# Performance work log

Hardware: AMD Instinct MI355X
Metric: run time of the kernel (lower is better)

## Reference

```python
import jax, jax.numpy as jnp
import numpy as np

DIM = 64
LEN = 256


def setup_inputs() -> dict:
    key = jax.random.key(0)
    ks = jax.random.split(key, 9)
    b, h, B = 4, 8, 16
    q = jax.random.normal(ks[0], (b, h, B, LEN, DIM), dtype=jnp.float32)
    k = jax.random.normal(ks[1], (b, h, B, LEN, DIM), dtype=jnp.float32)
    s = 1.0 / np.sqrt(DIM)
    Wq = jax.random.normal(ks[2], (1, DIM), dtype=jnp.float32) * s
    bq = jnp.ones((1,), dtype=jnp.float32)
    Wk = jax.random.normal(ks[3], (1, DIM), dtype=jnp.float32) * s
    bk = jnp.ones((1,), dtype=jnp.float32)
    sl = 1.0 / np.sqrt(LEN)
    W1 = jax.random.normal(ks[4], (1, LEN), dtype=jnp.float32) * sl
    W2a = jax.random.normal(ks[5], (LEN, LEN), dtype=jnp.float32) * sl
    W2b = jax.random.normal(ks[6], (1, LEN), dtype=jnp.float32) * sl
    return {"q": q, "k": k, "Wq": Wq, "bq": bq, "Wk": Wk, "bk": bk,
            "W1": W1, "W2a": W2a, "W2b": W2b}


def reference(q, k, Wq, bq, Wk, bk, W1, W2a, W2b):
    # Sigma_q/k: [b,h,B,L,1]
    Sigma_q = jnp.einsum('bhgid,od->bhgio', q, Wq) + bq
    Sigma_k = jnp.einsum('bhgjd,od->bhgjo', k, Wk) + bk
    # similarity: [b,h,B,L,L]
    sim = jnp.einsum('bhgid,bhgjd->bhgij', q, k)
    # outer product of the scalar projections: [b,h,B,L,L]
    Sigma = Sigma_q * jnp.swapaxes(Sigma_k, -1, -2)
    # zero the diagonal (sim - diag_embed(diag(sim)))
    eye = jnp.eye(sim.shape[-1], dtype=sim.dtype)
    sim_norm = sim * (1.0 - eye)
    # mlp1: Linear(L,1) over last axis -> [b,h,B,L]
    theta = jnp.einsum('bhgij,j->bhgi', sim_norm, W1[0])
    # mlp2: Linear(L,L) -> LeakyReLU(0.1) -> Linear(L,1) over axis i -> [b,h,B,1]
    hdn = jnp.einsum('bhgi,oi->bhgo', theta, W2a)
    hdn = jnp.where(hdn >= 0, hdn, 0.1 * hdn)
    theta = jnp.einsum('bhgi,oi->bhgo', hdn, W2b)[..., None]  # [b,h,B,1,1]
    sim = sim * Sigma
    attn = jax.nn.softmax(sim, axis=-1) * (sim > theta)
    return attn
```

## Files before the change

kernel.cpp:

```cpp
#include <hip/hip_runtime.h>
#include <math.h>

#define LL 256
#define DD 64

typedef __attribute__((ext_vector_type(8))) short bf16x8;
typedef __attribute__((ext_vector_type(4))) float f32x4;

static __device__ __forceinline__ unsigned short f2bf(float f) {
    union { float f; unsigned u; } v; v.f = f;
    unsigned r = v.u + 0x7fffu + ((v.u >> 16) & 1u);
    return (unsigned short)(r >> 16);
}
static __device__ __forceinline__ float bf2f(unsigned short h) {
    union { unsigned u; float f; } v; v.u = ((unsigned)h) << 16;
    return v.f;
}

__launch_bounds__(512, 2)
__global__ void fused_attn_mfma(const float* __restrict__ q,
                                const float* __restrict__ k,
                                const float* __restrict__ Wq,
                                const float* __restrict__ bq,
                                const float* __restrict__ Wk,
                                const float* __restrict__ bk,
                                const float* __restrict__ W1,
                                const float* __restrict__ W2a,
                                const float* __restrict__ W2b,
                                float* __restrict__ out)
{
    extern __shared__ char smc[];
    unsigned short* kHi = (unsigned short*)smc;
    unsigned short* kLo = (unsigned short*)(smc + 32768);
    float* sPq  = (float*)(smc + 65536);
    float* sPk  = sPq + 256;
    float* sPqk = sPk + 256;
    float* sTh  = sPqk + 256;
    float* sSq  = sTh + 256;
    float* sSk  = sSq + 256;
    float* kwred= sSk + 256;
    float* kw_s = kwred + 512;
    float* sRed = kw_s + 64;

    const int tid  = threadIdx.x;
    const int lane = tid & 63;
    const int wid  = tid >> 6;
    const int r16  = lane & 15;
    const int g4   = lane >> 4;
    const int rbase = wid * 32;
    const int gidx = blockIdx.x;
    const size_t gbase = (size_t)gidx * (LL * DD);
    const float* qg = q + gbase;
    const float4* q4 = (const float4*)qg;
    const float4* k4 = (const float4*)(k + gbase);

    float4 aq[2][2][2];
#pragma unroll
    for (int tr = 0; tr < 2; ++tr)
#pragma unroll
        for (int kk = 0; kk < 2; ++kk) {
            const float* p = qg + (rbase + tr * 16 + r16) * DD + kk * 32 + g4 * 8;
            aq[tr][kk][0] = ((const float4*)p)[0];
            aq[tr][kk][1] = ((const float4*)p)[1];
        }

    const int dc = tid & 15;
    const float4 wq4 = ((const float4*)Wq)[dc];
    const float4 wk4 = ((const float4*)Wk)[dc];
    float kw0 = 0.f, kw1 = 0.f, kw2 = 0.f, kw3 = 0.f;

#pragma unroll
    for (int it = 0; it < 8; ++it) {
        const int f = it * 512 + tid;
        const int j = f >> 4;
        const float4 vq = q4[f];
        const float4 vk = k4[f];

        const int sw = (j & 7) << 4;
        const int boff = j * 128 + ((dc * 8) ^ sw);
        const unsigned short h0 = f2bf(vk.x), h1 = f2bf(vk.y),
                             h2 = f2bf(vk.z), h3 = f2bf(vk.w);
        uint2 hv, lv;
        hv.x = (unsigned)h0 | ((unsigned)h1 << 16);
        hv.y = (unsigned)h2 | ((unsigned)h3 << 16);
        const unsigned short l0 = f2bf(vk.x - bf2f(h0)), l1 = f2bf(vk.y - bf2f(h1)),
                             l2 = f2bf(vk.z - bf2f(h2)), l3 = f2bf(vk.w - bf2f(h3));
        lv.x = (unsigned)l0 | ((unsigned)l1 << 16);
        lv.y = (unsigned)l2 | ((unsigned)l3 << 16);
        *(uint2*)((char*)kHi + boff) = hv;
        *(uint2*)((char*)kLo + boff) = lv;

        const float w1j = W1[j];
        kw0 += w1j * vk.x; kw1 += w1j * vk.y; kw2 += w1j * vk.z; kw3 += w1j * vk.w;

        float pq  = vq.x * wq4.x + vq.y * wq4.y + vq.z * wq4.z + vq.w * wq4.w;
        float pk  = vk.x * wk4.x + vk.y * wk4.y + vk.z * wk4.z + vk.w * wk4.w;
        float pqk = vq.x * vk.x + vq.y * vk.y + vq.z * vk.z + vq.w * vk.w;
#pragma unroll
        for (int m = 1; m < 16; m <<= 1) {
            pq  += __shfl_xor(pq,  m);
            pk  += __shfl_xor(pk,  m);
            pqk += __shfl_xor(pqk, m);
        }
        if (dc == 0) { sPq[j] = pq; sPk[j] = pk; sPqk[j] = pqk; }
    }
    kw0 += __shfl_xor(kw0, 16); kw0 += __shfl_xor(kw0, 32);
    kw1 += __shfl_xor(kw1, 16); kw1 += __shfl_xor(kw1, 32);
    kw2 += __shfl_xor(kw2, 16); kw2 += __shfl_xor(kw2, 32);
    kw3 += __shfl_xor(kw3, 16); kw3 += __shfl_xor(kw3, 32);
    if (lane < 16) {
        float4 kv; kv.x = kw0; kv.y = kw1; kv.z = kw2; kv.w = kw3;
        ((float4*)kwred)[wid * 16 + lane] = kv;
    }

    bf16x8 qhi[2][2], qlo[2][2];
#pragma unroll
    for (int tr = 0; tr < 2; ++tr)
#pragma unroll
        for (int kk = 0; kk < 2; ++kk) {
            const float fv[8] = {aq[tr][kk][0].x, aq[tr][kk][0].y, aq[tr][kk][0].z, aq[tr][kk][0].w,
                                 aq[tr][kk][1].x, aq[tr][kk][1].y, aq[tr][kk][1].z, aq[tr][kk][1].w};
#pragma unroll
            for (int e = 0; e < 8; ++e) {
                const unsigned short h = f2bf(fv[e]);
                qhi[tr][kk][e] = (short)h;
                qlo[tr][kk][e] = (short)f2bf(fv[e] - bf2f(h));
            }
        }

    __syncthreads();
    if (tid < 64) {
        float s = 0.f;
#pragma unroll
        for (int w = 0; w < 8; ++w) s += kwred[w * 64 + tid];
        kw_s[tid] = s;
    }
    __syncthreads();

    const float bq0 = bq[0], bk0 = bk[0];
#pragma unroll
    for (int tr = 0; tr < 2; ++tr) {
        const int row = rbase + tr * 16 + r16;
        float s = 0.f;
#pragma unroll
        for (int kk = 0; kk < 2; ++kk) {
            const int d0 = kk * 32 + g4 * 8;
#pragma unroll
            for (int e = 0; e < 8; ++e) {
                const float qf = bf2f((unsigned short)qhi[tr][kk][e]) +
                                 bf2f((unsigned short)qlo[tr][kk][e]);
                s += qf * kw_s[d0 + e];
            }
        }
        s += __shfl_xor(s, 16);
        s += __shfl_xor(s, 32);
        if (g4 == 0) {
            sTh[row] = s - W1[row] * sPqk[row];
            sSq[row] = sPq[row] + bq0;
            sSk[row] = sPk[row] + bk0;
        }
    }
    __syncthreads();

    {
        const int o = tid >> 1, ih = tid & 1;
        const float4* wrow = (const float4*)W2a + o * 64 + ih * 32;
        const float4* th4  = (const float4*)sTh + ih * 32;
        float h = 0.f;
#pragma unroll 8
        for (int c = 0; c < 32; ++c) {
            const float4 wv = wrow[c];
            const float4 tv = th4[c];
            h += wv.x * tv.x + wv.y * tv.y + wv.z * tv.z + wv.w * tv.w;
        }
        h += __shfl_xor(h, 1);
        float contrib = 0.f;
        if (ih == 0) {
            const float hl = (h >= 0.f) ? h : 0.1f * h;
            contrib = hl * W2b[o];
        }
#pragma unroll
        for (int m = 1; m < 64; m <<= 1) contrib += __shfl_xor(contrib, m);
        if (lane == 0) sRed[wid] = contrib;
    }
    __syncthreads();

    f32x4 acc[2][16];
#pragma unroll
    for (int tr = 0; tr < 2; ++tr)
#pragma unroll
        for (int ct = 0; ct < 16; ++ct)
            acc[tr][ct] = (f32x4){0.f, 0.f, 0.f, 0.f};

#pragma unroll
    for (int ct = 0; ct < 16; ++ct) {
        const int rowk = ct * 16 + r16;
        const int sw = (rowk & 7) << 4;
        const char* ph = (const char*)kHi + rowk * 128;
        const char* pl = (const char*)kLo + rowk * 128;
        const bf16x8 bh0 = *(const bf16x8*)(ph + ((g4 * 16) ^ sw));
        const bf16x8 bh1 = *(const bf16x8*)(ph + ((64 + g4 * 16) ^ sw));
        const bf16x8 bl0 = *(const bf16x8*)(pl + ((g4 * 16) ^ sw));
        const bf16x8 bl1 = *(const bf16x8*)(pl + ((64 + g4 * 16) ^ sw));
#pragma unroll
        for (int tr = 0; tr < 2; ++tr) {
            f32x4 c = acc[tr][ct];
            c = __builtin_amdgcn_mfma_f32_16x16x32_bf16(qhi[tr][0], bh0, c, 0, 0, 0);
            c = __builtin_amdgcn_mfma_f32_16x16x32_bf16(qhi[tr][1], bh1, c, 0, 0, 0);
            c = __builtin_amdgcn_mfma_f32_16x16x32_bf16(qhi[tr][0], bl0, c, 0, 0, 0);
            c = __builtin_amdgcn_mfma_f32_16x16x32_bf16(qhi[tr][1], bl1, c, 0, 0, 0);
            c = __builtin_amdgcn_mfma_f32_16x16x32_bf16(qlo[tr][0], bh0, c, 0, 0, 0);
            c = __builtin_amdgcn_mfma_f32_16x16x32_bf16(qlo[tr][1], bh1, c, 0, 0, 0);
            c = __builtin_amdgcn_mfma_f32_16x16x32_bf16(qlo[tr][0], bl0, c, 0, 0, 0);
            c = __builtin_amdgcn_mfma_f32_16x16x32_bf16(qlo[tr][1], bl1, c, 0, 0, 0);
            acc[tr][ct] = c;
        }
    }

    const float th_sc = sRed[0] + sRed[1] + sRed[2] + sRed[3] +
                        sRed[4] + sRed[5] + sRed[6] + sRed[7];
    float skv[16];
#pragma unroll
    for (int ct = 0; ct < 16; ++ct) skv[ct] = sSk[ct * 16 + r16];

    float* og = out + (size_t)gidx * (LL * LL);
#pragma unroll
    for (int tr = 0; tr < 2; ++tr) {
#pragma unroll
        for (int r = 0; r < 4; ++r) {
            const int row = rbase + tr * 16 + g4 * 4 + r;
            const float sq = sSq[row];
            float lg[16];
            float mx = -INFINITY;
#pragma unroll
            for (int ct = 0; ct < 16; ++ct) {
                lg[ct] = acc[tr][ct][r] * sq * skv[ct];
                mx = fmaxf(mx, lg[ct]);
            }
            mx = fmaxf(mx, __shfl_xor(mx, 1));
            mx = fmaxf(mx, __shfl_xor(mx, 2));
            mx = fmaxf(mx, __shfl_xor(mx, 4));
            mx = fmaxf(mx, __shfl_xor(mx, 8));
            float sum = 0.f;
#pragma unroll
            for (int ct = 0; ct < 16; ++ct) {
                const float pe = __expf(lg[ct] - mx);
                sum += pe;
                lg[ct] = (lg[ct] > th_sc) ? pe : 0.f;
            }
            sum += __shfl_xor(sum, 1);
            sum += __shfl_xor(sum, 2);
            sum += __shfl_xor(sum, 4);
            sum += __shfl_xor(sum, 8);
            const float rinv = 1.0f / sum;
#pragma unroll
            for (int ct = 0; ct < 16; ++ct)
                og[row * LL + ct * 16 + r16] = lg[ct] * rinv;
        }
    }
}

extern "C" void kernel_launch(void* const* d_in, const int* in_sizes, int n_in,
                              void* d_out, int out_size, void* d_ws, size_t ws_size,
                              hipStream_t stream) {
    const float* q   = (const float*)d_in[0];
    const float* k   = (const float*)d_in[1];
    const float* Wq  = (const float*)d_in[2];
    const float* bq  = (const float*)d_in[3];
    const float* Wk  = (const float*)d_in[4];
    const float* bk  = (const float*)d_in[5];
    const float* W1  = (const float*)d_in[6];
    const float* W2a = (const float*)d_in[7];
    const float* W2b = (const float*)d_in[8];
    float* out = (float*)d_out;

    const int ngroup = in_sizes[0] / (LL * DD);
    const size_t lds_bytes = 65536 + 2120 * sizeof(float);

    (void)hipFuncSetAttribute((const void*)fused_attn_mfma,
                              hipFuncAttributeMaxDynamicSharedMemorySize,
                              (int)lds_bytes);

    fused_attn_mfma<<<dim3(ngroup), dim3(512), lds_bytes, stream>>>(
        q, k, Wq, bq, Wk, bk, W1, W2a, W2b, out);
}
```

Measured before the change: 227.0 us.

## Split each group across four row-blocks and read K directly from global

Each group's 256 rows are now split across four 256-thread blocks of 64 rows each, giving four times as many blocks. The large LDS staging of K as bf16 hi/lo is removed; K is read from global/L2 and converted to bf16 inside the MFMA loop. The lo*lo MFMA term is dropped, going from 4 to 3 products per k-slice. Each block recomputes the per-group theta and projection prologue, so that work and the K reads are duplicated fourfold. In exchange, occupancy should rise because LDS use falls.

```diff
diff --git a/kernel.cpp b/kernel.cpp
--- a/kernel.cpp
+++ b/kernel.cpp
@@ -17,246 +17,192 @@
     return v.f;
 }
 
-__launch_bounds__(512, 2)
-__global__ void fused_attn_mfma(const float* __restrict__ q,
-                                const float* __restrict__ k,
-                                const float* __restrict__ Wq,
-                                const float* __restrict__ bq,
-                                const float* __restrict__ Wk,
-                                const float* __restrict__ bk,
-                                const float* __restrict__ W1,
-                                const float* __restrict__ W2a,
-                                const float* __restrict__ W2b,
-                                float* __restrict__ out)
+__launch_bounds__(256, 4)
+__global__ void fused_attn_v8(const float* __restrict__ q,
+                              const float* __restrict__ k,
+                              const float* __restrict__ Wq,
+                              const float* __restrict__ bq,
+                              const float* __restrict__ Wk,
+                              const float* __restrict__ bk,
+                              const float* __restrict__ W1,
+                              const float* __restrict__ W2a,
+                              const float* __restrict__ W2b,
+                              float* __restrict__ out,
+                              int ngroup)
 {
-    extern __shared__ char smc[];
-    unsigned short* kHi = (unsigned short*)smc;
-    unsigned short* kLo = (unsigned short*)(smc + 32768);
-    float* sPq  = (float*)(smc + 65536);
-    float* sPk  = sPq + 256;
-    float* sPqk = sPk + 256;
-    float* sTh  = sPqk + 256;
-    float* sSq  = sTh + 256;
-    float* sSk  = sSq + 256;
-    float* kwred= sSk + 256;
-    float* kw_s = kwred + 512;
-    float* sRed = kw_s + 64;
+    __shared__ float sPq[256];
+    __shared__ float sPk[256];
+    __shared__ float sPqk[256];
+    __shared__ float sTh[256];
+    __shared__ float kwred[4][64];
+    __shared__ float kw_s[64];
+    __shared__ float sRed[4];
 
     const int tid  = threadIdx.x;
     const int lane = tid & 63;
-    const int wid  = tid >> 6;
+    const int w    = tid >> 6;
     const int r16  = lane & 15;
     const int g4   = lane >> 4;
-    const int rbase = wid * 32;
-    const int gidx = blockIdx.x;
+
+    const int bid  = blockIdx.x;
+    const int gidx = bid % ngroup;
+    const int rb   = bid / ngroup;
+    const int row0 = rb * 64 + w * 16;
+
     const size_t gbase = (size_t)gidx * (LL * DD);
     const float* qg = q + gbase;
+    const float* kg = k + gbase;
     const float4* q4 = (const float4*)qg;
-    const float4* k4 = (const float4*)(k + gbase);
-
-    float4 aq[2][2][2];
-#pragma unroll
-    for (int tr = 0; tr < 2; ++tr)
-#pragma unroll
-        for (int kk = 0; kk < 2; ++kk) {
-            const float* p = qg + (rbase + tr * 16 + r16) * DD + kk * 32 + g4 * 8;
-            aq[tr][kk][0] = ((const float4*)p)[0];
-            aq[tr][kk][1] = ((const float4*)p)[1];
-        }
-
-    const int dc = tid & 15;
-    const float4 wq4 = ((const float4*)Wq)[dc];
-    const float4 wk4 = ((const float4*)Wk)[dc];
-    float kw0 = 0.f, kw1 = 0.f, kw2 = 0.f, kw3 = 0.f;
-
-#pragma unroll
-    for (int it = 0; it < 8; ++it) {
-        const int f = it * 512 + tid;
-        const int j = f >> 4;
-        const float4 vq = q4[f];
-        const float4 vk = k4[f];
-
-        const int sw = (j & 7) << 4;
-        const int boff = j * 128 + ((dc * 8) ^ sw);
-        const unsigned short h0 = f2bf(vk.x), h1 = f2bf(vk.y),
-                             h2 = f2bf(vk.z), h3 = f2bf(vk.w);
-        uint2 hv, lv;
-        hv.x = (unsigned)h0 | ((unsigned)h1 << 16);
-        hv.y = (unsigned)h2 | ((unsigned)h3 << 16);
-        const unsigned short l0 = f2bf(vk.x - bf2f(h0)), l1 = f2bf(vk.y - bf2f(h1)),
-                             l2 = f2bf(vk.z - bf2f(h2)), l3 = f2bf(vk.w - bf2f(h3));
-        lv.x = (unsigned)l0 | ((unsigned)l1 << 16);
-        lv.y = (unsigned)l2 | ((unsigned)l3 << 16);
-        *(uint2*)((char*)kHi + boff) = hv;
-        *(uint2*)((char*)kLo + boff) = lv;
-
-        const float w1j = W1[j];
-        kw0 += w1j * vk.x; kw1 += w1j * vk.y; kw2 += w1j * vk.z; kw3 += w1j * vk.w;
-
-        float pq  = vq.x * wq4.x + vq.y * wq4.y + vq.z * wq4.z + vq.w * wq4.w;
-        float pk  = vk.x * wk4.x + vk.y * wk4.y + vk.z * wk4.z + vk.w * wk4.w;
-        float pqk = vq.x * vk.x + vq.y * vk.y + vq.z * vk.z + vq.w * vk.w;
-#pragma unroll
-        for (int m = 1; m < 16; m <<= 1) {
-            pq  += __shfl_xor(pq,  m);
-            pk  += __shfl_xor(pk,  m);
-            pqk += __shfl_xor(pqk, m);
-        }
-        if (dc == 0) { sPq[j] = pq; sPk[j] = pk; sPqk[j] = pqk; }
-    }
-    kw0 += __shfl_xor(kw0, 16); kw0 += __shfl_xor(kw0, 32);
-    kw1 += __shfl_xor(kw1, 16); kw1 += __shfl_xor(kw1, 32);
-    kw2 += __shfl_xor(kw2, 16); kw2 += __shfl_xor(kw2, 32);
-    kw3 += __shfl_xor(kw3, 16); kw3 += __shfl_xor(kw3, 32);
-    if (lane < 16) {
-        float4 kv; kv.x = kw0; kv.y = kw1; kv.z = kw2; kv.w = kw3;
-        ((float4*)kwred)[wid * 16 + lane] = kv;
-    }
-
-    bf16x8 qhi[2][2], qlo[2][2];
-#pragma unroll
-    for (int tr = 0; tr < 2; ++tr)
-#pragma unroll
-        for (int kk = 0; kk < 2; ++kk) {
-            const float fv[8] = {aq[tr][kk][0].x, aq[tr][kk][0].y, aq[tr][kk][0].z, aq[tr][kk][0].w,
-                                 aq[tr][kk][1].x, aq[tr][kk][1].y, aq[tr][kk][1].z, aq[tr][kk][1].w};
-#pragma unroll
-            for (int e = 0; e < 8; ++e) {
-                const unsigned short h = f2bf(fv[e]);
-                qhi[tr][kk][e] = (short)h;
-                qlo[tr][kk][e] = (short)f2bf(fv[e] - bf2f(h));
-            }
-        }
-
-    __syncthreads();
-    if (tid < 64) {
+    const float4* k4 = (const float4*)kg;
+
+    float4 aq[2][2];
+#pragma unroll
+    for (int kk = 0; kk < 2; ++kk) {
+        const float* p = qg + (row0 + r16) * DD + kk * 32 + g4 * 8;
+        aq[kk][0] = ((const float4*)p)[0];
+        aq[kk][1] = ((const float4*)p)[1];
+    }
+
+    {
+        const float4* wq4 = (const float4*)Wq;
+        const float4* wk4 = (const float4*)Wk;
+        float pq = 0.f, pk = 0.f, pqk = 0.f;
+#pragma unroll
+        for (int it = 0; it < 16; ++it) {
+            const float4 vq = q4[tid * 16 + it];
+            const float4 vk = k4[tid * 16 + it];
+            const float4 a = wq4[it];
+            const float4 b = wk4[it];
+            pq  += vq.x * a.x + vq.y * a.y + vq.z * a.z + vq.w * a.w;
+            pk  += vk.x * b.x + vk.y * b.y + vk.z * b.z + vk.w * b.w;
+            pqk += vq.x * vk.x + vq.y * vk.y + vq.z * vk.z + vq.w * vk.w;
+        }
+        sPq[tid] = pq; sPk[tid] = pk; sPqk[tid] = pqk;
+    }
+
+    {
+        const int dd = tid & 63, jc = tid >> 6;
         float s = 0.f;
-#pragma unroll
-        for (int w = 0; w < 8; ++w) s += kwred[w * 64 + tid];
-        kw_s[tid] = s;
-    }
-    __syncthreads();
-
-    const float bq0 = bq[0], bk0 = bk[0];
-#pragma unroll
-    for (int tr = 0; tr < 2; ++tr) {
-        const int row = rbase + tr * 16 + r16;
+#pragma unroll 8
+        for (int j = jc * 64; j < jc * 64 + 64; ++j)
+            s += W1[j] * kg[j * DD + dd];
+        kwred[jc][dd] = s;
+    }
+    __syncthreads();
+    if (tid < 64)
+        kw_s[tid] = kwred[0][tid] + kwred[1][tid] + kwred[2][tid] + kwred[3][tid];
+    __syncthreads();
+
+    {
+        const float bq0 = bq[0], bk0 = bk[0];
+        const float4* kw4 = (const float4*)kw_s;
         float s = 0.f;
 #pragma unroll
-        for (int kk = 0; kk < 2; ++kk) {
-            const int d0 = kk * 32 + g4 * 8;
-#pragma unroll
-            for (int e = 0; e < 8; ++e) {
-                const float qf = bf2f((unsigned short)qhi[tr][kk][e]) +
-                                 bf2f((unsigned short)qlo[tr][kk][e]);
-                s += qf * kw_s[d0 + e];
-            }
-        }
-        s += __shfl_xor(s, 16);
-        s += __shfl_xor(s, 32);
-        if (g4 == 0) {
-            sTh[row] = s - W1[row] * sPqk[row];
-            sSq[row] = sPq[row] + bq0;
-            sSk[row] = sPk[row] + bk0;
-        }
-    }
-    __syncthreads();
-
-    {
-        const int o = tid >> 1, ih = tid & 1;
-        const float4* wrow = (const float4*)W2a + o * 64 + ih * 32;
-        const float4* th4  = (const float4*)sTh + ih * 32;
+        for (int it = 0; it < 16; ++it) {
+            const float4 vq = q4[tid * 16 + it];
+            const float4 kv = kw4[it];
+            s += vq.x * kv.x + vq.y * kv.y + vq.z * kv.z + vq.w * kv.w;
+        }
+        sTh[tid] = s - W1[tid] * sPqk[tid];
+        sPq[tid] += bq0;
+        sPk[tid] += bk0;
+    }
+    __syncthreads();
+
+    {
+        const float4* wrow = (const float4*)(W2a + tid * LL);
+        const float4* th4  = (const float4*)sTh;
         float h = 0.f;
 #pragma unroll 8
-        for (int c = 0; c < 32; ++c) {
+        for (int c = 0; c < 64; ++c) {
             const float4 wv = wrow[c];
             const float4 tv = th4[c];
             h += wv.x * tv.x + wv.y * tv.y + wv.z * tv.z + wv.w * tv.w;
         }
-        h += __shfl_xor(h, 1);
-        float contrib = 0.f;
-        if (ih == 0) {
-            const float hl = (h >= 0.f) ? h : 0.1f * h;
-            contrib = hl * W2b[o];
-        }
+        const float hl = (h >= 0.f) ? h : 0.1f * h;
+        float contrib = hl * W2b[tid];
 #pragma unroll
         for (int m = 1; m < 64; m <<= 1) contrib += __shfl_xor(contrib, m);
-        if (lane == 0) sRed[wid] = contrib;
-    }
-    __syncthreads();
-
-    f32x4 acc[2][16];
-#pragma unroll
-    for (int tr = 0; tr < 2; ++tr)
+        if (lane == 0) sRed[w] = contrib;
+    }
+    __syncthreads();
+    const float th_sc = sRed[0] + sRed[1] + sRed[2] + sRed[3];
+
+    bf16x8 qhi[2], qlo[2];
+#pragma unroll
+    for (int kk = 0; kk < 2; ++kk) {
+        const float fv[8] = {aq[kk][0].x, aq[kk][0].y, aq[kk][0].z, aq[kk][0].w,
+                             aq[kk][1].x, aq[kk][1].y, aq[kk][1].z, aq[kk][1].w};
+#pragma unroll
+        for (int e = 0; e < 8; ++e) {
+            const unsigned short h = f2bf(fv[e]);
+            qhi[kk][e] = (short)h;
+            qlo[kk][e] = (short)f2bf(fv[e] - bf2f(h));
+        }
+    }
+
+    f32x4 acc[16];
+#pragma unroll
+    for (int ct = 0; ct < 16; ++ct) acc[ct] = (f32x4){0.f, 0.f, 0.f, 0.f};
+
+#pragma unroll 4
+    for (int ct = 0; ct < 16; ++ct) {
+        const float* kp = kg + (ct * 16 + r16) * DD + g4 * 8;
+        f32x4 c = acc[ct];
+#pragma unroll
+        for (int kk = 0; kk < 2; ++kk) {
+            const float4 a = ((const float4*)(kp + kk * 32))[0];
+            const float4 b = ((const float4*)(kp + kk * 32))[1];
+            const float fv[8] = {a.x, a.y, a.z, a.w, b.x, b.y, b.z, b.w};
+            bf16x8 bh, bl;
+#pragma unroll
+            for (int e = 0; e < 8; ++e) {
+                const unsigned short h = f2bf(fv[e]);
+                bh[e] = (short)h;
+                bl[e] = (short)f2bf(fv[e] - bf2f(h));
+            }
+            c = __builtin_amdgcn_mfma_f32_16x16x32_bf16(qhi[kk], bh, c, 0, 0, 0);
+            c = __builtin_amdgcn_mfma_f32_16x16x32_bf16(qhi[kk], bl, c, 0, 0, 0);
+            c = __builtin_amdgcn_mfma_f32_16x16x32_bf16(qlo[kk], bh, c, 0, 0, 0);
+        }
+        acc[ct] = c;
+    }
+
+    float skv[16];
+#pragma unroll
+    for (int ct = 0; ct < 16; ++ct) skv[ct] = sPk[ct * 16 + r16];
+
+    float* og = out + (size_t)gidx * (LL * LL);
+#pragma unroll
+    for (int r = 0; r < 4; ++r) {
+        const int row = row0 + g4 * 4 + r;
+        const float sq = sPq[row];
+        float lg[16];
+        float mx = -INFINITY;
+#pragma unroll
+        for (int ct = 0; ct < 16; ++ct) {
+            lg[ct] = acc[ct][r] * sq * skv[ct];
+            mx = fmaxf(mx, lg[ct]);
+        }
+        mx = fmaxf(mx, __shfl_xor(mx, 1));
+        mx = fmaxf(mx, __shfl_xor(mx, 2));
+        mx = fmaxf(mx, __shfl_xor(mx, 4));
+        mx = fmaxf(mx, __shfl_xor(mx, 8));
+        float sum = 0.f;
+#pragma unroll
+        for (int ct = 0; ct < 16; ++ct) {
+            const float pe = __expf(lg[ct] - mx);
+            sum += pe;
+            lg[ct] = (lg[ct] > th_sc) ? pe : 0.f;
+        }
+        sum += __shfl_xor(sum, 1);
+        sum += __shfl_xor(sum, 2);
+        sum += __shfl_xor(sum, 4);
+        sum += __shfl_xor(sum, 8);
+        const float rinv = 1.0f / sum;
 #pragma unroll
         for (int ct = 0; ct < 16; ++ct)
-            acc[tr][ct] = (f32x4){0.f, 0.f, 0.f, 0.f};
-
-#pragma unroll
-    for (int ct = 0; ct < 16; ++ct) {
-        const int rowk = ct * 16 + r16;
-        const int sw = (rowk & 7) << 4;
-        const char* ph = (const char*)kHi + rowk * 128;
-        const char* pl = (const char*)kLo + rowk * 128;
-        const bf16x8 bh0 = *(const bf16x8*)(ph + ((g4 * 16) ^ sw));
-        const bf16x8 bh1 = *(const bf16x8*)(ph + ((64 + g4 * 16) ^ sw));
-        const bf16x8 bl0 = *(const bf16x8*)(pl + ((g4 * 16) ^ sw));
-        const bf16x8 bl1 = *(const bf16x8*)(pl + ((64 + g4 * 16) ^ sw));
-#pragma unroll
-        for (int tr = 0; tr < 2; ++tr) {
-            f32x4 c = acc[tr][ct];
-            c = __builtin_amdgcn_mfma_f32_16x16x32_bf16(qhi[tr][0], bh0, c, 0, 0, 0);
-            c = __builtin_amdgcn_mfma_f32_16x16x32_bf16(qhi[tr][1], bh1, c, 0, 0, 0);
-            c = __builtin_amdgcn_mfma_f32_16x16x32_bf16(qhi[tr][0], bl0, c, 0, 0, 0);
-            c = __builtin_amdgcn_mfma_f32_16x16x32_bf16(qhi[tr][1], bl1, c, 0, 0, 0);
-            c = __builtin_amdgcn_mfma_f32_16x16x32_bf16(qlo[tr][0], bh0, c, 0, 0, 0);
-            c = __builtin_amdgcn_mfma_f32_16x16x32_bf16(qlo[tr][1], bh1, c, 0, 0, 0);
-            c = __builtin_amdgcn_mfma_f32_16x16x32_bf16(qlo[tr][0], bl0, c, 0, 0, 0);
-            c = __builtin_amdgcn_mfma_f32_16x16x32_bf16(qlo[tr][1], bl1, c, 0, 0, 0);
-            acc[tr][ct] = c;
-        }
-    }
-
-    const float th_sc = sRed[0] + sRed[1] + sRed[2] + sRed[3] +
-                        sRed[4] + sRed[5] + sRed[6] + sRed[7];
-    float skv[16];
-#pragma unroll
-    for (int ct = 0; ct < 16; ++ct) skv[ct] = sSk[ct * 16 + r16];
-
-    float* og = out + (size_t)gidx * (LL * LL);
-#pragma unroll
-    for (int tr = 0; tr < 2; ++tr) {
-#pragma unroll
-        for (int r = 0; r < 4; ++r) {
-            const int row = rbase + tr * 16 + g4 * 4 + r;
-            const float sq = sSq[row];
-            float lg[16];
-            float mx = -INFINITY;
-#pragma unroll
-            for (int ct = 0; ct < 16; ++ct) {
-                lg[ct] = acc[tr][ct][r] * sq * skv[ct];
-                mx = fmaxf(mx, lg[ct]);
-            }
-            mx = fmaxf(mx, __shfl_xor(mx, 1));
-            mx = fmaxf(mx, __shfl_xor(mx, 2));
-            mx = fmaxf(mx, __shfl_xor(mx, 4));
-            mx = fmaxf(mx, __shfl_xor(mx, 8));
-            float sum = 0.f;
-#pragma unroll
-            for (int ct = 0; ct < 16; ++ct) {
-                const float pe = __expf(lg[ct] - mx);
-                sum += pe;
-                lg[ct] = (lg[ct] > th_sc) ? pe : 0.f;
-            }
-            sum += __shfl_xor(sum, 1);
-            sum += __shfl_xor(sum, 2);
-            sum += __shfl_xor(sum, 4);
-            sum += __shfl_xor(sum, 8);
-            const float rinv = 1.0f / sum;
-#pragma unroll
-            for (int ct = 0; ct < 16; ++ct)
-                og[row * LL + ct * 16 + r16] = lg[ct] * rinv;
-        }
+            og[row * LL + ct * 16 + r16] = lg[ct] * rinv;
     }
 }
 
@@ -275,12 +221,6 @@
     float* out = (float*)d_out;
 
     const int ngroup = in_sizes[0] / (LL * DD);
-    const size_t lds_bytes = 65536 + 2120 * sizeof(float);
-
-    (void)hipFuncSetAttribute((const void*)fused_attn_mfma,
-                              hipFuncAttributeMaxDynamicSharedMemorySize,
-                              (int)lds_bytes);
-
-    fused_attn_mfma<<<dim3(ngroup), dim3(512), lds_bytes, stream>>>(
-        q, k, Wq, bq, Wk, bk, W1, W2a, W2b, out);
-}
+    fused_attn_v8<<<dim3(ngroup * 4), dim3(256), 0, stream>>>(
+        q, k, Wq, bq, Wk, bk, W1, W2a, W2b, out, ngroup);
+}
```

Measured after the change: 462.2 us. 104% more time.
